# Kernel tuning notes

Measured on AMD Instinct MI355X. Metric: run time of the kernel, lower is better.

The kernel has to match this reference:

```python
import jax, jax.numpy as jnp
import numpy as np

DIM = 1024
NUM_HEAD = 16
DIM_HEAD = DIM // NUM_HEAD
RMS_EPS = 1.1920929e-07  # torch.finfo(float32).eps (nn.RMSNorm default eps=None)
EPS_LIN = 1e-6
THETA = 10000.0


def rmsnorm(x, g, eps=RMS_EPS):
    return x * jax.lax.rsqrt(jnp.mean(x * x, axis=-1, keepdims=True) + eps) * g


def rope_cos_sin(seq_len, dim_head, dtype=jnp.float32):
    inv_freq = 1.0 / (THETA ** (jnp.arange(0, dim_head, 2, dtype=dtype) / dim_head))
    t = jnp.arange(seq_len, dtype=dtype)
    freqs = jnp.outer(t, inv_freq)  # [L, dh//2]
    return jnp.cos(freqs), jnp.sin(freqs)


def apply_rope(t, cos, sin):
    # t: [b, h, L, dh]; pairs are (t[...,2i], t[...,2i+1]) viewed as complex
    tr = t[..., 0::2]
    ti = t[..., 1::2]
    out_r = tr * cos - ti * sin
    out_i = tr * sin + ti * cos
    return jnp.stack([out_r, out_i], axis=-1).reshape(t.shape)


def setup_inputs() -> dict:
    key = jax.random.key(0)
    ks = jax.random.split(key, 5)
    B, L = 4, 4096
    x = jax.random.normal(ks[0], (B, L, DIM), dtype=jnp.float32)
    Wqkv = jax.random.normal(ks[1], (3 * DIM, DIM), dtype=jnp.float32) * 0.02
    bqkv = jax.random.normal(ks[2], (3 * DIM,), dtype=jnp.float32) * 0.02
    gq = jnp.ones((DIM,), dtype=jnp.float32)
    gk = jnp.ones((DIM,), dtype=jnp.float32)
    Wout = jax.random.normal(ks[3], (DIM, DIM), dtype=jnp.float32) * 0.02
    bout = jax.random.normal(ks[4], (DIM,), dtype=jnp.float32) * 0.02
    gout = jnp.ones((DIM,), dtype=jnp.float32)
    return {"x": x, "Wqkv": Wqkv, "bqkv": bqkv, "gq": gq, "gk": gk,
            "Wout": Wout, "bout": bout, "gout": gout}


def reference(x, Wqkv, bqkv, gq, gk, Wout, bout, gout):
    B, L, D = x.shape
    qkv = x @ Wqkv.T + bqkv  # [B, L, 3D]
    q, k, v = jnp.split(qkv, 3, axis=-1)
    q = rmsnorm(q, gq)
    k = rmsnorm(k, gk)
    # b L (h d) -> b h L d
    split = lambda t: t.reshape(B, L, NUM_HEAD, DIM_HEAD).transpose(0, 2, 1, 3)
    q, k, v = split(q), split(k), split(v)
    cos, sin = rope_cos_sin(L, DIM_HEAD)  # start_pos = 0 (default)
    cos = cos[None, None]  # [1,1,L,dh//2]
    sin = sin[None, None]
    q = apply_rope(q, cos, sin)
    k = apply_rope(k, cos, sin)
    # linear attention: ReLU feature map + padded-value normalization trick
    qf = jax.nn.relu(q)
    kf = jax.nn.relu(k)
    vpad = jnp.concatenate([v, jnp.ones_like(v[..., :1])], axis=-1)  # pad_val=1.0
    vk = jnp.einsum('bhlp,bhld->bhpd', vpad, kf)       # [b,h,dh+1,dh]
    res = jnp.einsum('bhpd,bhld->bhlp', vk, qf)        # [b,h,L,dh+1]
    attn = res[..., :-1] / (res[..., -1:] + EPS_LIN)
    attn = attn.transpose(0, 2, 1, 3).reshape(B, L, D)  # b h L d -> b L (h d)
    out = rmsnorm(attn @ Wout.T + bout, gout)
    return out
```

## Files before the change

### kernel.cpp

```cpp
#include <hip/hip_runtime.h>
#include <stdint.h>

#define RMS_EPS 1.1920929e-07f
#define EPS_LIN 1e-6f

typedef __attribute__((ext_vector_type(8))) short bf16x8;
typedef __attribute__((ext_vector_type(4))) float f32x4;

__device__ __forceinline__ unsigned short f2bf(float f) {
  union { float f; unsigned int u; } v; v.f = f;
  unsigned int r = v.u + 0x7fffu + ((v.u >> 16) & 1u);
  return (unsigned short)(r >> 16);
}
__device__ __forceinline__ float bf2f(unsigned short s) {
  union { unsigned int u; float f; } v; v.u = ((unsigned int)s) << 16;
  return v.f;
}

__global__ __launch_bounds__(256) void k_f32_to_bf16(const float* __restrict__ src,
                                                     unsigned short* __restrict__ dst, int n) {
  int i = (blockIdx.x * 256 + threadIdx.x) * 4;
  if (i >= n) return;
  float4 v = *reinterpret_cast<const float4*>(src + i);
  ushort4 o = { f2bf(v.x), f2bf(v.y), f2bf(v.z), f2bf(v.w) };
  *reinterpret_cast<ushort4*>(dst + i) = o;
}

__global__ __launch_bounds__(256) void k_rope_table(float* __restrict__ cosT,
                                                    float* __restrict__ sinT) {
  int idx = blockIdx.x * 256 + threadIdx.x;
  if (idx >= 4096 * 32) return;
  int l = idx >> 5, i = idx & 31;
  float inv_freq = expf(-((float)(2 * i) / 64.0f) * logf(10000.0f));
  float ang = (float)l * inv_freq;
  cosT[idx] = cosf(ang);
  sinT[idx] = sinf(ang);
}

__device__ __forceinline__ void stage16(const unsigned short* g, unsigned short* lds_base,
                                        int lane) {
#if __has_builtin(__builtin_amdgcn_global_load_lds)
  __builtin_amdgcn_global_load_lds(
      (const __attribute__((address_space(1))) unsigned int*)g,
      (__attribute__((address_space(3))) unsigned int*)lds_base, 16, 0, 0);
#else
  *reinterpret_cast<uint4*>(lds_base + lane * 8) = *reinterpret_cast<const uint4*>(g);
#endif
}

__global__ __launch_bounds__(256) void k_gemm_bt(
    const unsigned short* __restrict__ A, const unsigned short* __restrict__ Bw,
    const float* __restrict__ bias, int M, int N, int K, int mode,
    unsigned short* __restrict__ qb, unsigned short* __restrict__ kb,
    unsigned short* __restrict__ vb, unsigned short* __restrict__ preb) {
  __shared__ unsigned short As[128 * 32];
  __shared__ unsigned short Bs[128 * 32];
  const int nt = N >> 7;
  const int bm = blockIdx.x / nt, bn = blockIdx.x % nt;
  const int m0 = bm << 7, n0 = bn << 7;
  const int t = threadIdx.x;
  const int wave = t >> 6, lane = t & 63;
  const int wr = wave >> 1, wc = wave & 1;
  const int lrow = lane >> 2, lcol = (lane & 3) * 8;

  const unsigned short* Ag0 = A + (size_t)(m0 + wave * 32 + lrow) * K + lcol;
  const unsigned short* Ag1 = Ag0 + (size_t)16 * K;
  const unsigned short* Bg0 = Bw + (size_t)(n0 + wave * 32 + lrow) * K + lcol;
  const unsigned short* Bg1 = Bg0 + (size_t)16 * K;
  unsigned short* Al0 = As + wave * 1024;
  unsigned short* Al1 = As + wave * 1024 + 512;
  unsigned short* Bl0 = Bs + wave * 1024;
  unsigned short* Bl1 = Bs + wave * 1024 + 512;

  f32x4 acc[4][4] = {};
  const int quad = lane >> 4, m16 = lane & 15;

  for (int k0 = 0; k0 < K; k0 += 32) {
    stage16(Ag0 + k0, Al0, lane);
    stage16(Ag1 + k0, Al1, lane);
    stage16(Bg0 + k0, Bl0, lane);
    stage16(Bg1 + k0, Bl1, lane);
    __syncthreads();
    bf16x8 fa[4], fb[4];
#pragma unroll
    for (int i = 0; i < 4; ++i)
      fa[i] = *reinterpret_cast<const bf16x8*>(As + (wr * 64 + i * 16 + m16) * 32 + quad * 8);
#pragma unroll
    for (int j = 0; j < 4; ++j)
      fb[j] = *reinterpret_cast<const bf16x8*>(Bs + (wc * 64 + j * 16 + m16) * 32 + quad * 8);
#pragma unroll
    for (int i = 0; i < 4; ++i)
#pragma unroll
      for (int j = 0; j < 4; ++j)
        acc[i][j] = __builtin_amdgcn_mfma_f32_16x16x32_bf16(fa[i], fb[j], acc[i][j], 0, 0, 0);
    __syncthreads();
  }

#pragma unroll
  for (int i = 0; i < 4; ++i) {
    int rbase = m0 + wr * 64 + i * 16 + quad * 4;
#pragma unroll
    for (int j = 0; j < 4; ++j) {
      int col = n0 + wc * 64 + j * 16 + m16;
      float bc = bias[col];
#pragma unroll
      for (int r = 0; r < 4; ++r) {
        int row = rbase + r;
        float val = acc[i][j][r] + bc;
        unsigned short bv = f2bf(val);
        if (mode == 0) {
          if (col < 1024) {
            qb[(size_t)row * 1024 + col] = bv;
          } else if (col < 2048) {
            kb[(size_t)row * 1024 + (col - 1024)] = bv;
          } else {
            int h = (col - 2048) >> 6, d = col & 63;
            int b = row >> 12, l = row & 4095;
            vb[(((size_t)(b * 16 + h)) * 4096 + l) * 64 + d] = bv;
          }
        } else {
          preb[(size_t)row * N + col] = bv;
        }
      }
    }
  }
}

__global__ __launch_bounds__(256) void k_qknorm(
    const unsigned short* __restrict__ qb, const unsigned short* __restrict__ kb,
    const float* __restrict__ gq, const float* __restrict__ gk,
    const float* __restrict__ cosT, const float* __restrict__ sinT,
    unsigned short* __restrict__ qfb, unsigned short* __restrict__ kfb) {
  const int row = blockIdx.x >> 1;
  const int which = blockIdx.x & 1;
  const int l = row & 4095;
  const int b = row >> 12;
  const int t = threadIdx.x;
  __shared__ float red[4];
  __shared__ float s_sc;
  const int d = t * 4;
  const int h = d >> 6;
  const int i0 = (d & 63) >> 1;
  const float c0 = cosT[l * 32 + i0], s0 = sinT[l * 32 + i0];
  const float c1 = cosT[l * 32 + i0 + 1], s1 = sinT[l * 32 + i0 + 1];
  const unsigned short* src = which ? kb : qb;
  const float* g = which ? gk : gq;
  unsigned short* dst = which ? kfb : qfb;
  ushort4 u = *reinterpret_cast<const ushort4*>(src + (size_t)row * 1024 + d);
  float v0 = bf2f(u.x), v1 = bf2f(u.y), v2 = bf2f(u.z), v3 = bf2f(u.w);
  float ss = v0 * v0 + v1 * v1 + v2 * v2 + v3 * v3;
#pragma unroll
  for (int off = 32; off; off >>= 1) ss += __shfl_down(ss, off, 64);
  if ((t & 63) == 0) red[t >> 6] = ss;
  __syncthreads();
  if (t == 0)
    s_sc = rsqrtf((red[0] + red[1] + red[2] + red[3]) * (1.0f / 1024.0f) + RMS_EPS);
  __syncthreads();
  const float sc = s_sc;
  float x0 = v0 * sc * g[d], x1 = v1 * sc * g[d + 1];
  float x2 = v2 * sc * g[d + 2], x3 = v3 * sc * g[d + 3];
  float r0 = x0 * c0 - x1 * s0, r1 = x0 * s0 + x1 * c0;
  float r2 = x2 * c1 - x3 * s1, r3 = x2 * s1 + x3 * c1;
  ushort4 o = { f2bf(fmaxf(r0, 0.f)), f2bf(fmaxf(r1, 0.f)),
                f2bf(fmaxf(r2, 0.f)), f2bf(fmaxf(r3, 0.f)) };
  *reinterpret_cast<ushort4*>(dst + (((size_t)(b * 16 + h)) * 4096 + l) * 64 + (d & 63)) = o;
}

__global__ __launch_bounds__(256) void k_vk(const unsigned short* __restrict__ vb,
                                            const unsigned short* __restrict__ kfb,
                                            float* __restrict__ vk) {
  const int bh = blockIdx.x >> 4;
  const int chunk = blockIdx.x & 15;
  const int t = threadIdx.x;
  const int wv = t >> 6, tx = t & 63;
  __shared__ float vt[64 * 64];
  __shared__ float kt[64 * 64];
  float acc[16] = {};
  float accD = 0.f;
  const int lb = chunk * 256;
  for (int tile = 0; tile < 4; ++tile) {
    const size_t rowbase = ((size_t)bh * 4096 + lb + tile * 64) * 64;
#pragma unroll
    for (int r = 0; r < 4; ++r) {
      int e = r * 1024 + t * 4;
      ushort4 uv = *reinterpret_cast<const ushort4*>(vb + rowbase + e);
      ushort4 uk = *reinterpret_cast<const ushort4*>(kfb + rowbase + e);
      float4 fv = { bf2f(uv.x), bf2f(uv.y), bf2f(uv.z), bf2f(uv.w) };
      float4 fk = { bf2f(uk.x), bf2f(uk.y), bf2f(uk.z), bf2f(uk.w) };
      *reinterpret_cast<float4*>(vt + e) = fv;
      *reinterpret_cast<float4*>(kt + e) = fk;
    }
    __syncthreads();
#pragma unroll 4
    for (int lp = 0; lp < 64; ++lp) {
      float kvv = kt[lp * 64 + tx];
      const float4* vr = reinterpret_cast<const float4*>(vt + lp * 64 + wv * 16);
      float4 v0 = vr[0], v1 = vr[1], v2 = vr[2], v3 = vr[3];
      acc[0] += v0.x * kvv;  acc[1] += v0.y * kvv;
      acc[2] += v0.z * kvv;  acc[3] += v0.w * kvv;
      acc[4] += v1.x * kvv;  acc[5] += v1.y * kvv;
      acc[6] += v1.z * kvv;  acc[7] += v1.w * kvv;
      acc[8] += v2.x * kvv;  acc[9] += v2.y * kvv;
      acc[10] += v2.z * kvv; acc[11] += v2.w * kvv;
      acc[12] += v3.x * kvv; acc[13] += v3.y * kvv;
      acc[14] += v3.z * kvv; acc[15] += v3.w * kvv;
      accD += kvv;
    }
    __syncthreads();
  }
  float* dst = vk + (size_t)bh * 65 * 64;
#pragma unroll
  for (int pp = 0; pp < 16; ++pp) atomicAdd(dst + (wv * 16 + pp) * 64 + tx, acc[pp]);
  if (wv == 0) atomicAdd(dst + 64 * 64 + tx, accD);
}

__global__ __launch_bounds__(256) void k_res(const unsigned short* __restrict__ qfb,
                                             const float* __restrict__ vk,
                                             unsigned short* __restrict__ attnb) {
  const int bh = blockIdx.x >> 5;
  const int lt = (blockIdx.x & 31) << 7;
  const int b = bh >> 4, h = bh & 15;
  const int t = threadIdx.x;
  const int wave = t >> 6, lane = t & 63;
  __shared__ unsigned short Aq[128 * 64];
  __shared__ unsigned short Bv[64 * 64];
  __shared__ float vkD[64];
  __shared__ float invden[128];

  const unsigned short* Ag = qfb + ((size_t)bh * 4096 + lt) * 64;
#pragma unroll
  for (int s = 0; s < 4; ++s)
    stage16(Ag + wave * 2048 + s * 512 + lane * 8, Aq + wave * 2048 + s * 512, lane);

  const float* vsrc = vk + (size_t)bh * 65 * 64;
  {
    int base = t * 16;
#pragma unroll
    for (int c = 0; c < 4; ++c) {
      float4 f = *reinterpret_cast<const float4*>(vsrc + base + c * 4);
      ushort4 o = { f2bf(f.x), f2bf(f.y), f2bf(f.z), f2bf(f.w) };
      *reinterpret_cast<ushort4*>(Bv + base + c * 4) = o;
    }
  }
  if (t < 64) vkD[t] = vsrc[64 * 64 + t];
  __syncthreads();

  f32x4 acc[2][4] = {};
  const int quad = lane >> 4, m16 = lane & 15;
#pragma unroll
  for (int step = 0; step < 2; ++step) {
    bf16x8 fa[2], fb[4];
#pragma unroll
    for (int i = 0; i < 2; ++i)
      fa[i] = *reinterpret_cast<const bf16x8*>(Aq + (wave * 32 + i * 16 + m16) * 64 +
                                               step * 32 + quad * 8);
#pragma unroll
    for (int j = 0; j < 4; ++j)
      fb[j] = *reinterpret_cast<const bf16x8*>(Bv + (j * 16 + m16) * 64 +
                                               step * 32 + quad * 8);
#pragma unroll
    for (int i = 0; i < 2; ++i)
#pragma unroll
      for (int j = 0; j < 4; ++j)
        acc[i][j] = __builtin_amdgcn_mfma_f32_16x16x32_bf16(fa[i], fb[j], acc[i][j], 0, 0, 0);
  }

  {
    const unsigned short* qr = Aq + (t >> 1) * 64 + (t & 1) * 32;
    const float* vd = vkD + (t & 1) * 32;
    float ds = 0.f;
#pragma unroll
    for (int c = 0; c < 4; ++c) {
      bf16x8 qv = *reinterpret_cast<const bf16x8*>(qr + c * 8);
#pragma unroll
      for (int j = 0; j < 8; ++j)
        ds += bf2f((unsigned short)qv[j]) * vd[c * 8 + j];
    }
    ds += __shfl_xor(ds, 1, 64);
    if ((t & 1) == 0) invden[t >> 1] = 1.0f / (ds + EPS_LIN);
  }
  __syncthreads();

#pragma unroll
  for (int i = 0; i < 2; ++i) {
#pragma unroll
    for (int r = 0; r < 4; ++r) {
      int row = wave * 32 + i * 16 + quad * 4 + r;
      float inv = invden[row];
      unsigned short* dst = attnb + ((size_t)(b * 4096 + lt + row)) * 1024 + h * 64;
#pragma unroll
      for (int j = 0; j < 4; ++j)
        dst[j * 16 + m16] = f2bf(acc[i][j][r] * inv);
    }
  }
}

__global__ __launch_bounds__(256) void k_outnorm(const unsigned short* __restrict__ preb,
                                                 const float* __restrict__ gout,
                                                 float* __restrict__ out) {
  const int row = blockIdx.x;
  const int t = threadIdx.x;
  __shared__ float red[4];
  __shared__ float s_sc;
  ushort4 u = *reinterpret_cast<const ushort4*>(preb + (size_t)row * 1024 + t * 4);
  float v0 = bf2f(u.x), v1 = bf2f(u.y), v2 = bf2f(u.z), v3 = bf2f(u.w);
  float ss = v0 * v0 + v1 * v1 + v2 * v2 + v3 * v3;
#pragma unroll
  for (int off = 32; off; off >>= 1) ss += __shfl_down(ss, off, 64);
  if ((t & 63) == 0) red[t >> 6] = ss;
  __syncthreads();
  if (t == 0) s_sc = rsqrtf((red[0] + red[1] + red[2] + red[3]) * (1.0f / 1024.0f) + RMS_EPS);
  __syncthreads();
  const float sc = s_sc;
  const int d = t * 4;
  float4 o = { v0 * sc * gout[d], v1 * sc * gout[d + 1],
               v2 * sc * gout[d + 2], v3 * sc * gout[d + 3] };
  *reinterpret_cast<float4*>(out + (size_t)row * 1024 + d) = o;
}

#define OFF_XB     0ull
#define OFF_WQKVB  33554432ull
#define OFF_WOUTB  39845888ull
#define OFF_QB     41943040ull
#define OFF_KB     75497472ull
#define OFF_VB     109051904ull
#define OFF_QFB    142606336ull
#define OFF_KFB    176160768ull
#define OFF_VK     209715200ull
#define OFF_ATTNB  210780160ull
#define OFF_COST   244334592ull
#define OFF_SINT   244858880ull
#define WS_NEEDED  245383168ull

extern "C" void kernel_launch(void* const* d_in, const int* in_sizes, int n_in,
                              void* d_out, int out_size, void* d_ws, size_t ws_size,
                              hipStream_t stream) {
  const float* x    = (const float*)d_in[0];
  const float* Wqkv = (const float*)d_in[1];
  const float* bqkv = (const float*)d_in[2];
  const float* gq   = (const float*)d_in[3];
  const float* gk   = (const float*)d_in[4];
  const float* Wout = (const float*)d_in[5];
  const float* bout = (const float*)d_in[6];
  const float* gout = (const float*)d_in[7];

  if (ws_size < WS_NEEDED) return;

  char* ws = (char*)d_ws;
  unsigned short* xb    = (unsigned short*)(ws + OFF_XB);
  unsigned short* wqkvb = (unsigned short*)(ws + OFF_WQKVB);
  unsigned short* woutb = (unsigned short*)(ws + OFF_WOUTB);
  unsigned short* qb    = (unsigned short*)(ws + OFF_QB);
  unsigned short* kb    = (unsigned short*)(ws + OFF_KB);
  unsigned short* vb    = (unsigned short*)(ws + OFF_VB);
  unsigned short* qfb   = (unsigned short*)(ws + OFF_QFB);
  unsigned short* kfb   = (unsigned short*)(ws + OFF_KFB);
  float*          vkbuf = (float*)(ws + OFF_VK);
  unsigned short* attnb = (unsigned short*)(ws + OFF_ATTNB);
  float*          cosT  = (float*)(ws + OFF_COST);
  float*          sinT  = (float*)(ws + OFF_SINT);
  unsigned short* preb  = (unsigned short*)(ws + OFF_QB);

  k_f32_to_bf16<<<16384, 256, 0, stream>>>(x, xb, 16777216);
  k_f32_to_bf16<<<3072, 256, 0, stream>>>(Wqkv, wqkvb, 3145728);
  k_f32_to_bf16<<<1024, 256, 0, stream>>>(Wout, woutb, 1048576);
  k_rope_table<<<512, 256, 0, stream>>>(cosT, sinT);

  k_gemm_bt<<<128 * 24, 256, 0, stream>>>(xb, wqkvb, bqkv, 16384, 3072, 1024, 0,
                                          qb, kb, vb, nullptr);
  k_qknorm<<<32768, 256, 0, stream>>>(qb, kb, gq, gk, cosT, sinT, qfb, kfb);

  hipMemsetAsync(vkbuf, 0, 64 * 65 * 64 * sizeof(float), stream);
  k_vk<<<1024, 256, 0, stream>>>(vb, kfb, vkbuf);
  k_res<<<2048, 256, 0, stream>>>(qfb, vkbuf, attnb);

  k_gemm_bt<<<128 * 8, 256, 0, stream>>>(attnb, woutb, bout, 16384, 1024, 1024, 1,
                                         nullptr, nullptr, nullptr, preb);
  k_outnorm<<<16384, 256, 0, stream>>>(preb, gout, (float*)d_out);
}
```

Baseline: 459.9 us.

## Double GEMM K-tile to 64 with XOR-swizzled LDS layout

The bf16 GEMM now stages a 64-wide K slice per iteration instead of 32, which halves the number of barrier pairs per K loop. The LDS tiles use an XOR swizzle on the 16-byte chunk index so that MFMA fragment reads avoid bank conflicts. Fragment offsets are precomputed, and launch bounds request 3 blocks per CU. The cost is LDS per block doubling to 32 KB and higher register pressure from the precomputed pointers and offsets.

```diff
diff --git a/kernel.cpp b/kernel.cpp
--- a/kernel.cpp
+++ b/kernel.cpp
@@ -48,51 +48,73 @@
 #endif
 }
 
-__global__ __launch_bounds__(256) void k_gemm_bt(
+__global__ __launch_bounds__(256, 3) void k_gemm_bt(
     const unsigned short* __restrict__ A, const unsigned short* __restrict__ Bw,
     const float* __restrict__ bias, int M, int N, int K, int mode,
     unsigned short* __restrict__ qb, unsigned short* __restrict__ kb,
     unsigned short* __restrict__ vb, unsigned short* __restrict__ preb) {
-  __shared__ unsigned short As[128 * 32];
-  __shared__ unsigned short Bs[128 * 32];
+  __shared__ unsigned short As[128 * 64];
+  __shared__ unsigned short Bs[128 * 64];
   const int nt = N >> 7;
   const int bm = blockIdx.x / nt, bn = blockIdx.x % nt;
   const int m0 = bm << 7, n0 = bn << 7;
   const int t = threadIdx.x;
   const int wave = t >> 6, lane = t & 63;
   const int wr = wave >> 1, wc = wave & 1;
-  const int lrow = lane >> 2, lcol = (lane & 3) * 8;
-
-  const unsigned short* Ag0 = A + (size_t)(m0 + wave * 32 + lrow) * K + lcol;
-  const unsigned short* Ag1 = Ag0 + (size_t)16 * K;
-  const unsigned short* Bg0 = Bw + (size_t)(n0 + wave * 32 + lrow) * K + lcol;
-  const unsigned short* Bg1 = Bg0 + (size_t)16 * K;
-  unsigned short* Al0 = As + wave * 1024;
-  unsigned short* Al1 = As + wave * 1024 + 512;
-  unsigned short* Bl0 = Bs + wave * 1024;
-  unsigned short* Bl1 = Bs + wave * 1024 + 512;
+  const int quad = lane >> 4, m16 = lane & 15;
+
+  const unsigned short* ApS[4];
+  const unsigned short* BpS[4];
+  unsigned short* AlS[4];
+  unsigned short* BlS[4];
+#pragma unroll
+  for (int s = 0; s < 4; ++s) {
+    int u = wave * 256 + s * 64 + lane;
+    int row = u >> 3;
+    int ku = (u & 7) ^ (row & 7);
+    ApS[s] = A + (size_t)(m0 + row) * K + ku * 8;
+    BpS[s] = Bw + (size_t)(n0 + row) * K + ku * 8;
+    AlS[s] = As + (size_t)(wave * 256 + s * 64) * 8;
+    BlS[s] = Bs + (size_t)(wave * 256 + s * 64) * 8;
+  }
+
+  int offA[4][2], offB[4][2];
+#pragma unroll
+  for (int i = 0; i < 4; ++i) {
+    int rowA = wr * 64 + i * 16 + m16;
+    int rowB = wc * 64 + i * 16 + m16;
+#pragma unroll
+    for (int ks = 0; ks < 2; ++ks) {
+      int kuf = ks * 4 + quad;
+      offA[i][ks] = (rowA * 8 + (kuf ^ (rowA & 7))) * 8;
+      offB[i][ks] = (rowB * 8 + (kuf ^ (rowB & 7))) * 8;
+    }
+  }
 
   f32x4 acc[4][4] = {};
-  const int quad = lane >> 4, m16 = lane & 15;
-
-  for (int k0 = 0; k0 < K; k0 += 32) {
-    stage16(Ag0 + k0, Al0, lane);
-    stage16(Ag1 + k0, Al1, lane);
-    stage16(Bg0 + k0, Bl0, lane);
-    stage16(Bg1 + k0, Bl1, lane);
+
+  for (int k0 = 0; k0 < K; k0 += 64) {
+#pragma unroll
+    for (int s = 0; s < 4; ++s) {
+      stage16(ApS[s] + k0, AlS[s], lane);
+      stage16(BpS[s] + k0, BlS[s], lane);
+    }
     __syncthreads();
-    bf16x8 fa[4], fb[4];
-#pragma unroll
-    for (int i = 0; i < 4; ++i)
-      fa[i] = *reinterpret_cast<const bf16x8*>(As + (wr * 64 + i * 16 + m16) * 32 + quad * 8);
-#pragma unroll
-    for (int j = 0; j < 4; ++j)
-      fb[j] = *reinterpret_cast<const bf16x8*>(Bs + (wc * 64 + j * 16 + m16) * 32 + quad * 8);
-#pragma unroll
-    for (int i = 0; i < 4; ++i)
+#pragma unroll
+    for (int ks = 0; ks < 2; ++ks) {
+      bf16x8 fa[4], fb[4];
+#pragma unroll
+      for (int i = 0; i < 4; ++i)
+        fa[i] = *reinterpret_cast<const bf16x8*>(As + offA[i][ks]);
 #pragma unroll
       for (int j = 0; j < 4; ++j)
-        acc[i][j] = __builtin_amdgcn_mfma_f32_16x16x32_bf16(fa[i], fb[j], acc[i][j], 0, 0, 0);
+        fb[j] = *reinterpret_cast<const bf16x8*>(Bs + offB[j][ks]);
+#pragma unroll
+      for (int i = 0; i < 4; ++i)
+#pragma unroll
+        for (int j = 0; j < 4; ++j)
+          acc[i][j] = __builtin_amdgcn_mfma_f32_16x16x32_bf16(fa[i], fb[j], acc[i][j], 0, 0, 0);
+    }
     __syncthreads();
   }
 
```

Result: faster. 407.9 us (-11.3%).
